# Optimization experiments

Measured on AMD Instinct MI355X. Metric: run time of the kernel, lower is better.

## Reference

```python
import jax, jax.numpy as jnp
import numpy as np

NUM_ITEM = 80000
NUM_USER = 20000
N = NUM_ITEM + NUM_USER
E = 1_000_000
DIM_FEAT = 64
USER_DIM = 128
DIM_ID = 64
SLOPE = 0.01  # F.leaky_relu default negative_slope


def setup_inputs() -> dict:
    key = jax.random.key(0)
    ks = jax.random.split(key, 16)
    s = 0.05
    # self-loop-free random edge list (torch code removes self loops)
    src = jax.random.randint(ks[0], (E,), 0, N)
    off = jax.random.randint(ks[1], (E,), 1, N)
    dst = (src + off) % N
    edge_index = jnp.stack([src, dst]).astype(jnp.int32)
    return {
        "features": jax.random.normal(ks[2], (NUM_ITEM, DIM_FEAT), jnp.float32),
        "user_features": jax.random.normal(ks[3], (NUM_USER, USER_DIM), jnp.float32),
        "id_embedding_weight": jax.random.normal(ks[4], (N, DIM_ID), jnp.float32) * s,
        "user_mlp_w": jax.random.normal(ks[5], (DIM_FEAT, USER_DIM), jnp.float32) * s,
        "user_mlp_b": jnp.zeros((DIM_FEAT,), jnp.float32),
        "gat1_w": jax.random.normal(ks[6], (DIM_FEAT, DIM_FEAT), jnp.float32) * s,
        "lin1_w": jax.random.normal(ks[7], (DIM_ID, DIM_FEAT), jnp.float32) * s,
        "lin1_b": jnp.zeros((DIM_ID,), jnp.float32),
        "g1_w": jax.random.normal(ks[8], (DIM_ID, DIM_FEAT), jnp.float32) * s,
        "g1_b": jnp.zeros((DIM_ID,), jnp.float32),
        "gat2_w": jax.random.normal(ks[9], (DIM_ID, DIM_ID), jnp.float32) * s,
        "lin2_w": jax.random.normal(ks[10], (DIM_ID, DIM_ID), jnp.float32) * s,
        "lin2_b": jnp.zeros((DIM_ID,), jnp.float32),
        "g2_w": jax.random.normal(ks[11], (DIM_ID, DIM_ID), jnp.float32) * s,
        "g2_b": jnp.zeros((DIM_ID,), jnp.float32),
        "edge_index": edge_index,
    }


def leaky_relu(x):
    return jnp.where(x >= 0, x, SLOPE * x)


def graph_gat(x, W, src, dst):
    """GraphGAT layer (MGAT-style): x@W, inner-product attention with
    degree-based sigmoid gate, edge softmax over target nodes, scatter-add."""
    n = x.shape[0]
    xw = x @ W                                   # [N, d_out]
    x_i = xw[dst]                                # gathered target feats [E, d]
    x_j = xw[src]                                # gathered source feats [E, d]
    inner = jnp.sum(x_i * x_j, axis=-1)          # [E]
    deg = jnp.zeros((n,), xw.dtype).at[src].add(1.0)
    dinv = deg[src] ** -0.5                      # deg[src] >= 1 by construction
    gate = jax.nn.sigmoid(dinv * inner)
    logits = inner * gate
    # segment softmax over destination index (PyG softmax)
    m = jax.ops.segment_max(logits, dst, num_segments=n)
    m = jnp.where(jnp.isfinite(m), m, 0.0)
    e = jnp.exp(logits - m[dst])
    z = jax.ops.segment_sum(e, dst, num_segments=n)
    attn = e / (z[dst] + 1e-16)
    msg = x_j * attn[:, None]                    # [E, d]
    return jnp.zeros_like(xw).at[dst].add(msg)   # scatter-add aggr


def reference(features, user_features, id_embedding_weight,
              user_mlp_w, user_mlp_b,
              gat1_w, lin1_w, lin1_b, g1_w, g1_b,
              gat2_w, lin2_w, lin2_b, g2_w, g2_b,
              edge_index):
    src, dst = edge_index[0], edge_index[1]
    user = jnp.tanh(user_features @ user_mlp_w.T + user_mlp_b)
    x = jnp.concatenate([features, user], axis=0)          # [N, dim_feat]
    nrm = jnp.linalg.norm(x, axis=-1, keepdims=True)
    x = x / jnp.maximum(nrm, 1e-12)                        # F.normalize

    # hop 1
    h = leaky_relu(graph_gat(x, gat1_w, src, dst))
    x_hat = leaky_relu(x @ lin1_w.T + lin1_b) + id_embedding_weight
    x1 = leaky_relu(h @ g1_w.T + g1_b + x_hat)

    # hop 2
    h = leaky_relu(graph_gat(x1, gat2_w, src, dst))
    x_hat = leaky_relu(x1 @ lin2_w.T + lin2_b) + id_embedding_weight
    x2 = leaky_relu(h @ g2_w.T + g2_b + x_hat)

    return jnp.concatenate([x1, x2], axis=1)               # [N, 2*dim_id]
```

## Files before the change

kernel.cpp:

```cpp
#include <hip/hip_runtime.h>
#include <hip/hip_bf16.h>
#include <hip/hip_fp16.h>

#define N_ITEM 80000
#define N_USER 20000
#define NN     100000
#define NE     1000000
#define SCAN_T 1024
#define SCAN_TILES ((NN + SCAN_T - 1) / SCAN_T)

typedef __hip_bfloat16 bf16;

__device__ __forceinline__ float b2f(bf16 v) { return __bfloat162float(v); }
__device__ __forceinline__ bf16  f2b(float v) { return __float2bfloat16(v); }
__device__ __forceinline__ float bits2f(unsigned short h) {
    return __uint_as_float(((unsigned)h) << 16);
}
__device__ __forceinline__ float leaky(float v) { return v >= 0.f ? v : 0.01f * v; }

template<typename T>
__device__ __forceinline__ float ldT(const void* p, size_t i);
template<> __device__ __forceinline__ float ldT<float>(const void* p, size_t i) {
    return ((const float*)p)[i];
}
template<> __device__ __forceinline__ float ldT<bf16>(const void* p, size_t i) {
    return b2f(((const bf16*)p)[i]);
}
template<typename T>
__device__ __forceinline__ float4 ldT4(const void* p, size_t i);
template<> __device__ __forceinline__ float4 ldT4<float>(const void* p, size_t i) {
    return *(const float4*)((const float*)p + i);
}
template<> __device__ __forceinline__ float4 ldT4<bf16>(const void* p, size_t i) {
    ushort4 u = *(const ushort4*)((const unsigned short*)p + i);
    return make_float4(bits2f(u.x), bits2f(u.y), bits2f(u.z), bits2f(u.w));
}
template<typename T>
__device__ __forceinline__ void stT4(void* p, size_t i, float4 v);
template<> __device__ __forceinline__ void stT4<float>(void* p, size_t i, float4 v) {
    *(float4*)((float*)p + i) = v;
}
template<> __device__ __forceinline__ void stT4<bf16>(void* p, size_t i, float4 v) {
    bf16 b0 = f2b(v.x), b1 = f2b(v.y), b2 = f2b(v.z), b3 = f2b(v.w);
    ushort4 u = make_ushort4(*(unsigned short*)&b0, *(unsigned short*)&b1,
                             *(unsigned short*)&b2, *(unsigned short*)&b3);
    *(ushort4*)((unsigned short*)p + i) = u;
}
__device__ __forceinline__ float4 ld4f(const float* p, size_t i) {
    return *(const float4*)(p + i);
}
__device__ __forceinline__ float4 ld4b(const unsigned short* p, size_t i) {
    ushort4 u = *(const ushort4*)(p + i);
    return make_float4(bits2f(u.x), bits2f(u.y), bits2f(u.z), bits2f(u.w));
}
__device__ __forceinline__ void st4b(unsigned short* p, size_t i, float4 v) {
    bf16 b0 = f2b(v.x), b1 = f2b(v.y), b2 = f2b(v.z), b3 = f2b(v.w);
    ushort4 u = make_ushort4(*(unsigned short*)&b0, *(unsigned short*)&b1,
                             *(unsigned short*)&b2, *(unsigned short*)&b3);
    *(ushort4*)(p + i) = u;
}
__device__ __forceinline__ float4 ld4h(const unsigned short* p, size_t i) {
    ushort4 u = *(const ushort4*)(p + i);
    __half h0, h1, h2, h3;
    *(unsigned short*)&h0 = u.x; *(unsigned short*)&h1 = u.y;
    *(unsigned short*)&h2 = u.z; *(unsigned short*)&h3 = u.w;
    return make_float4(__half2float(h0), __half2float(h1),
                       __half2float(h2), __half2float(h3));
}
__device__ __forceinline__ void st4h(unsigned short* p, size_t i, float4 v) {
    __half h0 = __float2half(v.x), h1 = __float2half(v.y);
    __half h2 = __float2half(v.z), h3 = __float2half(v.w);
    ushort4 u = make_ushort4(*(unsigned short*)&h0, *(unsigned short*)&h1,
                             *(unsigned short*)&h2, *(unsigned short*)&h3);
    *(ushort4*)(p + i) = u;
}

__device__ __forceinline__ float wred(float v) {
    for (int o = 32; o; o >>= 1) v += __shfl_xor(v, o, 64);
    return v;
}
__device__ __forceinline__ float gred16(float v) {
    for (int o = 8; o; o >>= 1) v += __shfl_xor(v, o, 64);
    return v;
}
__device__ __forceinline__ int wscan(int v, int lane) {
    for (int o = 1; o < 64; o <<= 1) {
        int t = __shfl_up(v, o, 64);
        v += (lane >= o) ? t : 0;
    }
    return v;
}

__global__ void k_detect(const unsigned short* __restrict__ w, int* __restrict__ mode) {
    __shared__ int cnt[256];
    int bad = 0;
    for (int i = threadIdx.x; i < 4096; i += 256) {
        unsigned e = (w[i] >> 7) & 0xFFu;
        bad += (e == 0u || e == 0xFFu) ? 1 : 0;
    }
    cnt[threadIdx.x] = bad;
    __syncthreads();
    if (threadIdx.x == 0) {
        int t = 0;
        for (int k = 0; k < 256; k++) t += cnt[k];
        mode[0] = (t > 0) ? 1 : 0;
    }
}

__global__ void k_prep_w(const void* umw, const void* lw1, const void* gw1,
                         const void* lw2, const void* gw2,
                         float* umwT, float* wT, const int* mode) {
    int t = blockIdx.x * 256 + threadIdx.x;
    bool f32m = (*mode != 0);
    if (t < 8192) {
        int j = t >> 7, k = t & 127;
        float v = f32m ? ldT<float>(umw, t) : ldT<bf16>(umw, t);
        umwT[k * 64 + j] = v;
    } else {
        int u = t - 8192;
        int m = u >> 12;
        int r = u & 4095;
        int j = r >> 6, k = r & 63;
        const void* srcp = (m == 0) ? lw1 : (m == 1) ? gw1 : (m == 2) ? lw2 : gw2;
        float v = f32m ? ldT<float>(srcp, r) : ldT<bf16>(srcp, r);
        wT[m * 4096 + k * 64 + j] = v;
    }
}

__global__ void k_deg(const int* __restrict__ src, const int* __restrict__ dst,
                      int* __restrict__ deg, int* __restrict__ cnt) {
    int e = blockIdx.x * blockDim.x + threadIdx.x;
    if (e < NE) {
        atomicAdd(&deg[src[e]], 1);
        atomicAdd(&cnt[dst[e]], 1);
    }
}

__global__ void k_scan_sum(const int* __restrict__ cnt, const int* __restrict__ deg,
                           float* __restrict__ dinv, int* __restrict__ tsum) {
    __shared__ int wsum[16];
    int i = blockIdx.x * SCAN_T + threadIdx.x;
    int lane = threadIdx.x & 63, wid = threadIdx.x >> 6;
    int v = (i < NN) ? cnt[i] : 0;
    if (i < NN) dinv[i] = rsqrtf((float)max(deg[i], 1));
    float s = wred((float)v);
    if (lane == 0) wsum[wid] = (int)s;
    __syncthreads();
    if (threadIdx.x == 0) {
        int t = 0;
        #pragma unroll
        for (int k = 0; k < 16; k++) t += wsum[k];
        tsum[blockIdx.x] = t;
    }
}

__global__ void k_scan_tiles(const int* __restrict__ tsum, int* __restrict__ toff) {
    __shared__ int wsum[16];
    int lane = threadIdx.x & 63, wid = threadIdx.x >> 6;
    int v = (threadIdx.x < SCAN_TILES) ? tsum[threadIdx.x] : 0;
    int inc = wscan(v, lane);
    if (lane == 63) wsum[wid] = inc;
    __syncthreads();
    if (wid == 0) {
        int ws = (lane < 16) ? wsum[lane] : 0;
        int wi = wscan(ws, lane);
        if (lane < 16) wsum[lane] = wi - ws;
    }
    __syncthreads();
    if (threadIdx.x < SCAN_TILES) toff[threadIdx.x] = inc - v + wsum[wid];
}

__global__ void k_scan_out(const int* __restrict__ cnt, const int* __restrict__ toff,
                           int* __restrict__ csr_off, int* __restrict__ cursor) {
    __shared__ int wsum[16];
    int i = blockIdx.x * SCAN_T + threadIdx.x;
    int lane = threadIdx.x & 63, wid = threadIdx.x >> 6;
    int v = (i < NN) ? cnt[i] : 0;
    int inc = wscan(v, lane);
    if (lane == 63) wsum[wid] = inc;
    __syncthreads();
    if (wid == 0) {
        int ws = (lane < 16) ? wsum[lane] : 0;
        int wi = wscan(ws, lane);
        if (lane < 16) wsum[lane] = wi - ws;
    }
    __syncthreads();
    int excl = inc - v + wsum[wid] + toff[blockIdx.x];
    if (i < NN) { csr_off[i] = excl; cursor[i] = excl; }
    if (i == NN - 1) csr_off[NN] = excl + v;
}

__global__ void k_scatter(const int* __restrict__ src, const int* __restrict__ dst,
                          int* __restrict__ cursor, int* __restrict__ csr_src) {
    int e = blockIdx.x * blockDim.x + threadIdx.x;
    if (e < NE) {
        int pos = atomicAdd(&cursor[dst[e]], 1);
        csr_src[pos] = src[e];
    }
}

template<typename T>
__device__ __forceinline__ void front_items_body(float4* __restrict__ gsW,
                                                 float4* __restrict__ gsL,
                                                 const void* __restrict__ feat,
                                                 const void* __restrict__ Wg,
                                                 const float* __restrict__ lT,
                                                 const void* __restrict__ lb,
                                                 const void* __restrict__ id_emb,
                                                 unsigned short* __restrict__ xw,
                                                 unsigned short* __restrict__ xhat) {
    int lane = threadIdx.x & 63, wid = threadIdx.x >> 6;
    int sl = lane & 15;
    int i = blockIdx.x * 16 + (wid << 2) + (lane >> 4);
    #pragma unroll
    for (int t = 0; t < 4; t++) {
        int idx = threadIdx.x + t * 256;
        gsW[idx] = ldT4<T>(Wg, (size_t)idx * 4);
        gsL[idx] = ld4f(lT, (size_t)idx * 4);
    }
    size_t rb = (size_t)i * 64 + sl * 4;
    float4 v = ldT4<T>(feat, rb);
    float ss = gred16(v.x * v.x + v.y * v.y + v.z * v.z + v.w * v.w);
    float inv = 1.f / fmaxf(sqrtf(ss), 1e-12f);
    float4 xv = make_float4(v.x * inv, v.y * inv, v.z * inv, v.w * inv);
    float4 lb4 = ldT4<T>(lb, sl * 4);
    float4 id4 = ldT4<T>(id_emb, rb);
    __syncthreads();
    float4 accw = make_float4(0.f, 0.f, 0.f, 0.f);
    float4 accl = make_float4(0.f, 0.f, 0.f, 0.f);
    int gbase = lane & 48;
    #pragma unroll
    for (int kk = 0; kk < 16; kk++) {
        int srcl = gbase | kk;
        float xb[4];
        xb[0] = __shfl(xv.x, srcl, 64);
        xb[1] = __shfl(xv.y, srcl, 64);
        xb[2] = __shfl(xv.z, srcl, 64);
        xb[3] = __shfl(xv.w, srcl, 64);
        #pragma unroll
        for (int q = 0; q < 4; q++) {
            int wb = (kk * 4 + q) * 16 + sl;
            float4 w4 = gsW[wb];
            float4 l4 = gsL[wb];
            accw.x += xb[q] * w4.x; accw.y += xb[q] * w4.y;
            accw.z += xb[q] * w4.z; accw.w += xb[q] * w4.w;
            accl.x += xb[q] * l4.x; accl.y += xb[q] * l4.y;
            accl.z += xb[q] * l4.z; accl.w += xb[q] * l4.w;
        }
    }
    st4b(xw, rb, accw);
    float4 xh;
    xh.x = leaky(accl.x + lb4.x) + id4.x;
    xh.y = leaky(accl.y + lb4.y) + id4.y;
    xh.z = leaky(accl.z + lb4.z) + id4.z;
    xh.w = leaky(accl.w + lb4.w) + id4.w;
    st4h(xhat, rb, xh);
}
__global__ void k_front_items(const void* feat, const void* Wg, const float* lT,
                              const void* lb, const void* id_emb,
                              unsigned short* xw, unsigned short* xhat,
                              const int* mode) {
    __shared__ float4 gsW[1024];
    __shared__ float4 gsL[1024];
    if (*mode) front_items_body<float>(gsW, gsL, feat, Wg, lT, lb, id_emb, xw, xhat);
    else       front_items_body<bf16>(gsW, gsL, feat, Wg, lT, lb, id_emb, xw, xhat);
}

template<typename T>
__device__ __forceinline__ void front_users_body(float4* __restrict__ gs,
                                                 const void* __restrict__ uf,
                                                 const float* __restrict__ umwT,
                                                 const void* __restrict__ umb,
                                                 const void* __restrict__ Wg,
                                                 const float* __restrict__ lT,
                                                 const void* __restrict__ lb,
                                                 const void* __restrict__ id_emb,
                                                 unsigned short* __restrict__ xw,
                                                 unsigned short* __restrict__ xhat) {
    int lane = threadIdx.x & 63, wid = threadIdx.x >> 6;
    int sl = lane & 15;
    int u = blockIdx.x * 16 + (wid << 2) + (lane >> 4);
    int i = N_ITEM + u;
    int gbase = lane & 48;
    #pragma unroll
    for (int t = 0; t < 8; t++) {
        int idx = threadIdx.x + t * 256;
        gs[idx] = ld4f(umwT, (size_t)idx * 4);
    }
    __syncthreads();
    size_t ub = (size_t)u * 128;
    float4 acc = ldT4<T>(umb, sl * 4);
    #pragma unroll 4
    for (int k = 0; k < 128; k++) {
        float ufk = ldT<T>(uf, ub + k);
        float4 w4 = gs[k * 16 + sl];
        acc.x += ufk * w4.x; acc.y += ufk * w4.y;
        acc.z += ufk * w4.z; acc.w += ufk * w4.w;
    }
    float4 v = make_float4(tanhf(acc.x), tanhf(acc.y), tanhf(acc.z), tanhf(acc.w));
    float ss = gred16(v.x * v.x + v.y * v.y + v.z * v.z + v.w * v.w);
    float inv = 1.f / fmaxf(sqrtf(ss), 1e-12f);
    float4 xv = make_float4(v.x * inv, v.y * inv, v.z * inv, v.w * inv);
    __syncthreads();
    #pragma unroll
    for (int t = 0; t < 4; t++) {
        int idx = threadIdx.x + t * 256;
        gs[idx] = ldT4<T>(Wg, (size_t)idx * 4);
        gs[idx + 1024] = ld4f(lT, (size_t)idx * 4);
    }
    size_t rb = (size_t)i * 64 + sl * 4;
    float4 lb4 = ldT4<T>(lb, sl * 4);
    float4 id4 = ldT4<T>(id_emb, rb);
    __syncthreads();
    float4 accw = make_float4(0.f, 0.f, 0.f, 0.f);
    float4 accl = make_float4(0.f, 0.f, 0.f, 0.f);
    #pragma unroll
    for (int kk = 0; kk < 16; kk++) {
        int srcl = gbase | kk;
        float xb[4];
        xb[0] = __shfl(xv.x, srcl, 64);
        xb[1] = __shfl(xv.y, srcl, 64);
        xb[2] = __shfl(xv.z, srcl, 64);
        xb[3] = __shfl(xv.w, srcl, 64);
        #pragma unroll
        for (int q = 0; q < 4; q++) {
            int wb = (kk * 4 + q) * 16 + sl;
            float4 w4 = gs[wb];
            float4 l4 = gs[wb + 1024];
            accw.x += xb[q] * w4.x; accw.y += xb[q] * w4.y;
            accw.z += xb[q] * w4.z; accw.w += xb[q] * w4.w;
            accl.x += xb[q] * l4.x; accl.y += xb[q] * l4.y;
            accl.z += xb[q] * l4.z; accl.w += xb[q] * l4.w;
        }
    }
    st4b(xw, rb, accw);
    float4 xh;
    xh.x = leaky(accl.x + lb4.x) + id4.x;
    xh.y = leaky(accl.y + lb4.y) + id4.y;
    xh.z = leaky(accl.z + lb4.z) + id4.z;
    xh.w = leaky(accl.w + lb4.w) + id4.w;
    st4h(xhat, rb, xh);
}
__global__ void k_front_users(const void* uf, const float* umwT, const void* umb,
                              const void* Wg, const float* lT, const void* lb,
                              const void* id_emb,
                              unsigned short* xw, unsigned short* xhat,
                              const int* mode) {
    __shared__ float4 gs[2048];
    if (*mode) front_users_body<float>(gs, uf, umwT, umb, Wg, lT, lb,
                                       id_emb, xw, xhat);
    else       front_users_body<bf16>(gs, uf, umwT, umb, Wg, lT, lb,
                                      id_emb, xw, xhat);
}

template<typename T>
__device__ __forceinline__ void pre_body(float4* __restrict__ gsW,
                                         float4* __restrict__ gsL,
                                         const float* __restrict__ xin,
                                         const void* __restrict__ Wg,
                                         const float* __restrict__ lT,
                                         const void* __restrict__ lb,
                                         const void* __restrict__ id_emb,
                                         unsigned short* __restrict__ xw,
                                         unsigned short* __restrict__ xhat) {
    int lane = threadIdx.x & 63, wid = threadIdx.x >> 6;
    int sl = lane & 15;
    int i = blockIdx.x * 16 + (wid << 2) + (lane >> 4);
    #pragma unroll
    for (int t = 0; t < 4; t++) {
        int idx = threadIdx.x + t * 256;
        gsW[idx] = ldT4<T>(Wg, (size_t)idx * 4);
        gsL[idx] = ld4f(lT, (size_t)idx * 4);
    }
    size_t rb = (size_t)i * 64 + sl * 4;
    float4 xv = ld4f(xin, rb);
    float4 lb4 = ldT4<T>(lb, sl * 4);
    float4 id4 = ldT4<T>(id_emb, rb);
    __syncthreads();
    float4 accw = make_float4(0.f, 0.f, 0.f, 0.f);
    float4 accl = make_float4(0.f, 0.f, 0.f, 0.f);
    int gbase = lane & 48;
    #pragma unroll
    for (int kk = 0; kk < 16; kk++) {
        int srcl = gbase | kk;
        float xb[4];
        xb[0] = __shfl(xv.x, srcl, 64);
        xb[1] = __shfl(xv.y, srcl, 64);
        xb[2] = __shfl(xv.z, srcl, 64);
        xb[3] = __shfl(xv.w, srcl, 64);
        #pragma unroll
        for (int q = 0; q < 4; q++) {
            int wb = (kk * 4 + q) * 16 + sl;
            float4 w4 = gsW[wb];
            float4 l4 = gsL[wb];
            accw.x += xb[q] * w4.x; accw.y += xb[q] * w4.y;
            accw.z += xb[q] * w4.z; accw.w += xb[q] * w4.w;
            accl.x += xb[q] * l4.x; accl.y += xb[q] * l4.y;
            accl.z += xb[q] * l4.z; accl.w += xb[q] * l4.w;
        }
    }
    st4b(xw, rb, accw);
    float4 xh;
    xh.x = leaky(accl.x + lb4.x) + id4.x;
    xh.y = leaky(accl.y + lb4.y) + id4.y;
    xh.z = leaky(accl.z + lb4.z) + id4.z;
    xh.w = leaky(accl.w + lb4.w) + id4.w;
    st4h(xhat, rb, xh);
}
__global__ void k_pre(const float* xin, const void* Wg, const float* lT,
                      const void* lb, const void* id_emb,
                      unsigned short* xw, unsigned short* xhat, const int* mode) {
    __shared__ float4 gsW[1024];
    __shared__ float4 gsL[1024];
    if (*mode) pre_body<float>(gsW, gsL, xin, Wg, lT, lb, id_emb, xw, xhat);
    else       pre_body<bf16>(gsW, gsL, xin, Wg, lT, lb, id_emb, xw, xhat);
}

template<typename T>
__device__ __forceinline__ void gat_body(float4* __restrict__ gs,
                                         const unsigned short* __restrict__ xw,
                                         const unsigned short* __restrict__ xhat,
                                         const int* __restrict__ csr_off,
                                         const int* __restrict__ csr_src,
                                         const float* __restrict__ dinv,
                                         const float* __restrict__ gTg,
                                         const void* gb,
                                         float* __restrict__ xnext, void* out,
                                         int off_out) {
    int lane = threadIdx.x & 63, wid = threadIdx.x >> 6;
    int sl = lane & 15;
    int i = blockIdx.x * 16 + (wid << 2) + (lane >> 4);
    size_t rb = (size_t)i * 64 + sl * 4;
    #pragma unroll
    for (int t = 0; t < 4; t++)
        gs[threadIdx.x + t * 256] = ((const float4*)gTg)[threadIdx.x + t * 256];

    float4 xd = ld4b(xw, rb);
    int e0 = csr_off[i], e1 = csr_off[i + 1];
    int cnt = e1 - e0;
    float m = -1e30f, l = 0.f;
    float4 acc = make_float4(0.f, 0.f, 0.f, 0.f);
    float4 xsA = make_float4(0.f, 0.f, 0.f, 0.f), xsB = xsA;
    float dA = 1.f, dB = 1.f;
    if (cnt > 0) {
        int s0 = csr_src[e0];
        xsA = ld4b(xw, (size_t)s0 * 64 + sl * 4);
        dA = dinv[s0];
    }
    if (cnt > 1) {
        int s1 = csr_src[e0 + 1];
        xsB = ld4b(xw, (size_t)s1 * 64 + sl * 4);
        dB = dinv[s1];
    }
    for (int t = 0; t < cnt; ++t) {
        float4 xs = xsA; float dv = dA;
        xsA = xsB; dA = dB;
        if (t + 2 < cnt) {
            int sn = csr_src[e0 + t + 2];
            xsB = ld4b(xw, (size_t)sn * 64 + sl * 4);
            dB = dinv[sn];
        }
        float p = xd.x * xs.x + xd.y * xs.y + xd.z * xs.z + xd.w * xs.w;
        float inner = gred16(p);
        float gate = 1.f / (1.f + __expf(-dv * inner));
        float logit = inner * gate;
        float mn = fmaxf(m, logit);
        float sc = __expf(m - mn);
        float w  = __expf(logit - mn);
        acc.x = acc.x * sc + w * xs.x;
        acc.y = acc.y * sc + w * xs.y;
        acc.z = acc.z * sc + w * xs.z;
        acc.w = acc.w * sc + w * xs.w;
        l = l * sc + w;
        m = mn;
    }
    float linv = 1.f / (l + 1e-16f);
    float4 hv = make_float4(leaky(acc.x * linv), leaky(acc.y * linv),
                            leaky(acc.z * linv), leaky(acc.w * linv));
    __syncthreads();
    float4 accg = make_float4(0.f, 0.f, 0.f, 0.f);
    int gbase = lane & 48;
    #pragma unroll
    for (int kk = 0; kk < 16; kk++) {
        int srcl = gbase | kk;
        float hb[4];
        hb[0] = __shfl(hv.x, srcl, 64);
        hb[1] = __shfl(hv.y, srcl, 64);
        hb[2] = __shfl(hv.z, srcl, 64);
        hb[3] = __shfl(hv.w, srcl, 64);
        #pragma unroll
        for (int q = 0; q < 4; q++) {
            float4 g4 = gs[(kk * 4 + q) * 16 + sl];
            accg.x += hb[q] * g4.x; accg.y += hb[q] * g4.y;
            accg.z += hb[q] * g4.z; accg.w += hb[q] * g4.w;
        }
    }
    float4 gb4 = ldT4<T>(gb, sl * 4);
    float4 xh4 = ld4h(xhat, rb);
    float4 xn;
    xn.x = leaky(accg.x + gb4.x + xh4.x);
    xn.y = leaky(accg.y + gb4.y + xh4.y);
    xn.z = leaky(accg.z + gb4.z + xh4.z);
    xn.w = leaky(accg.w + gb4.w + xh4.w);
    if (xnext) *(float4*)(xnext + rb) = xn;
    stT4<T>(out, (size_t)i * 128 + off_out + sl * 4, xn);
}
__global__ void k_gat(const unsigned short* xw, const unsigned short* xhat,
                      const int* csr_off, const int* csr_src, const float* dinv,
                      const float* gTg, const void* gb,
                      float* xnext, void* out, int off_out, const int* mode) {
    __shared__ float4 gs[1024];
    if (*mode) gat_body<float>(gs, xw, xhat, csr_off, csr_src, dinv, gTg, gb,
                               xnext, out, off_out);
    else       gat_body<bf16>(gs, xw, xhat, csr_off, csr_src, dinv, gTg, gb,
                              xnext, out, off_out);
}

extern "C" void kernel_launch(void* const* d_in, const int* in_sizes, int n_in,
                              void* d_out, int out_size, void* d_ws, size_t ws_size,
                              hipStream_t stream) {
    const void* feat   = d_in[0];
    const void* uf     = d_in[1];
    const void* id_emb = d_in[2];
    const void* umw    = d_in[3];
    const void* umb    = d_in[4];
    const void* gat1   = d_in[5];
    const void* lin1b  = d_in[7];
    const void* g1b    = d_in[9];
    const void* gat2   = d_in[10];
    const void* lin2b  = d_in[12];
    const void* g2b    = d_in[14];
    const int*  ei     = (const int*)d_in[15];
    const int* src = ei;
    const int* dst = ei + NE;

    int*      mode   = (int*)d_ws;
    int*      deg    = (int*)((char*)d_ws + 16);
    int*      cnt    = deg + NN;
    int*      cursor = cnt + NN;
    int*      csr_off = cursor + NN;
    int*      tsum   = csr_off + NN + 16;
    int*      toff   = tsum + 128;
    float*    dinv   = (float*)(toff + 128);
    float*    umwT   = dinv + NN;
    float*    wT     = umwT + 8192;
    int*      csr_src = (int*)(wT + 4 * 4096);
    float*    buf0   = (float*)(csr_src + NE);
    float*    buf2   = buf0 + (size_t)NN * 64;
    unsigned short* xwb   = (unsigned short*)(buf2 + (size_t)NN * 64);
    unsigned short* xhath = xwb + (size_t)NN * 64;

    k_detect<<<1, 256, 0, stream>>>((const unsigned short*)feat, mode);
    k_prep_w<<<96, 256, 0, stream>>>(umw, d_in[6], d_in[8], d_in[11], d_in[13],
                                     umwT, wT, mode);
    hipMemsetAsync(deg, 0, 2 * NN * 4, stream);
    k_deg<<<(NE + 255) / 256, 256, 0, stream>>>(src, dst, deg, cnt);
    k_scan_sum<<<SCAN_TILES, SCAN_T, 0, stream>>>(cnt, deg, dinv, tsum);
    k_scan_tiles<<<1, SCAN_T, 0, stream>>>(tsum, toff);
    k_scan_out<<<SCAN_TILES, SCAN_T, 0, stream>>>(cnt, toff, csr_off, cursor);
    k_scatter<<<(NE + 255) / 256, 256, 0, stream>>>(src, dst, cursor, csr_src);

    const float* lT1 = wT;
    const float* gT1 = wT + 4096;
    const float* lT2 = wT + 8192;
    const float* gT2 = wT + 12288;

    int nb = NN / 16;

    k_front_items<<<N_ITEM / 16, 256, 0, stream>>>(feat, gat1, lT1, lin1b,
                                                   id_emb, xwb, xhath, mode);
    k_front_users<<<N_USER / 16, 256, 0, stream>>>(uf, umwT, umb, gat1, lT1,
                                                   lin1b, id_emb, xwb, xhath,
                                                   mode);
    k_gat<<<nb, 256, 0, stream>>>(xwb, xhath, csr_off, csr_src, dinv,
                                  gT1, g1b, buf2, d_out, 0, mode);
    k_pre<<<nb, 256, 0, stream>>>(buf2, gat2, lT2, lin2b, id_emb,
                                  xwb, xhath, mode);
    k_gat<<<nb, 256, 0, stream>>>(xwb, xhath, csr_off, csr_src, dinv,
                                  gT2, g2b, nullptr, d_out, 64, mode);
}
```

Baseline: 558.9 us.

## Fuse hop-2 pre-projection into hop-1 GAT kernel with fp16 weights in LDS

The separate pre kernel, which read the hop-1 output x1 from an fp32 buffer, is folded into the first GAT kernel. That kernel now computes x1·gat2 and the lin2 projection from registers, using fp16 copies of both weights staged in shared memory. This removes one launch and the fp32 write and read of x1. Separate ping-pong buffers avoid overwriting xw and xhat while other blocks still read them. In exchange the fused kernel uses more LDS and registers, and the fp16 weights add small rounding error.

```diff
diff --git a/kernel.cpp b/kernel.cpp
--- a/kernel.cpp
+++ b/kernel.cpp
@@ -17,6 +17,10 @@
     return __uint_as_float(((unsigned)h) << 16);
 }
 __device__ __forceinline__ float leaky(float v) { return v >= 0.f ? v : 0.01f * v; }
+__device__ __forceinline__ unsigned short f2h(float v) {
+    __half h = __float2half(v);
+    return *(unsigned short*)&h;
+}
 
 template<typename T>
 __device__ __forceinline__ float ldT(const void* p, size_t i);
@@ -59,19 +63,18 @@
                              *(unsigned short*)&b2, *(unsigned short*)&b3);
     *(ushort4*)(p + i) = u;
 }
-__device__ __forceinline__ float4 ld4h(const unsigned short* p, size_t i) {
-    ushort4 u = *(const ushort4*)(p + i);
+__device__ __forceinline__ float4 cvt4h(ushort4 u) {
     __half h0, h1, h2, h3;
     *(unsigned short*)&h0 = u.x; *(unsigned short*)&h1 = u.y;
     *(unsigned short*)&h2 = u.z; *(unsigned short*)&h3 = u.w;
     return make_float4(__half2float(h0), __half2float(h1),
                        __half2float(h2), __half2float(h3));
 }
+__device__ __forceinline__ float4 ld4h(const unsigned short* p, size_t i) {
+    return cvt4h(*(const ushort4*)(p + i));
+}
 __device__ __forceinline__ void st4h(unsigned short* p, size_t i, float4 v) {
-    __half h0 = __float2half(v.x), h1 = __float2half(v.y);
-    __half h2 = __float2half(v.z), h3 = __float2half(v.w);
-    ushort4 u = make_ushort4(*(unsigned short*)&h0, *(unsigned short*)&h1,
-                             *(unsigned short*)&h2, *(unsigned short*)&h3);
+    ushort4 u = make_ushort4(f2h(v.x), f2h(v.y), f2h(v.z), f2h(v.w));
     *(ushort4*)(p + i) = u;
 }
 
@@ -108,15 +111,17 @@
 }
 
 __global__ void k_prep_w(const void* umw, const void* lw1, const void* gw1,
-                         const void* lw2, const void* gw2,
-                         float* umwT, float* wT, const int* mode) {
+                         const void* lw2, const void* gw2, const void* gat2,
+                         float* umwT, float* wT,
+                         unsigned short* wg2h, unsigned short* lt2h,
+                         const int* mode) {
     int t = blockIdx.x * 256 + threadIdx.x;
     bool f32m = (*mode != 0);
     if (t < 8192) {
         int j = t >> 7, k = t & 127;
         float v = f32m ? ldT<float>(umw, t) : ldT<bf16>(umw, t);
         umwT[k * 64 + j] = v;
-    } else {
+    } else if (t < 24576) {
         int u = t - 8192;
         int m = u >> 12;
         int r = u & 4095;
@@ -124,6 +129,11 @@
         const void* srcp = (m == 0) ? lw1 : (m == 1) ? gw1 : (m == 2) ? lw2 : gw2;
         float v = f32m ? ldT<float>(srcp, r) : ldT<bf16>(srcp, r);
         wT[m * 4096 + k * 64 + j] = v;
+        if (m == 2) lt2h[k * 64 + j] = f2h(v);
+    } else {
+        int r = t - 24576;
+        float v = f32m ? ldT<float>(gat2, r) : ldT<bf16>(gat2, r);
+        wg2h[r] = f2h(v);
     }
 }
 
@@ -354,86 +364,33 @@
 }
 
 template<typename T>
-__device__ __forceinline__ void pre_body(float4* __restrict__ gsW,
-                                         float4* __restrict__ gsL,
-                                         const float* __restrict__ xin,
-                                         const void* __restrict__ Wg,
-                                         const float* __restrict__ lT,
-                                         const void* __restrict__ lb,
-                                         const void* __restrict__ id_emb,
-                                         unsigned short* __restrict__ xw,
-                                         unsigned short* __restrict__ xhat) {
-    int lane = threadIdx.x & 63, wid = threadIdx.x >> 6;
-    int sl = lane & 15;
-    int i = blockIdx.x * 16 + (wid << 2) + (lane >> 4);
-    #pragma unroll
-    for (int t = 0; t < 4; t++) {
-        int idx = threadIdx.x + t * 256;
-        gsW[idx] = ldT4<T>(Wg, (size_t)idx * 4);
-        gsL[idx] = ld4f(lT, (size_t)idx * 4);
-    }
-    size_t rb = (size_t)i * 64 + sl * 4;
-    float4 xv = ld4f(xin, rb);
-    float4 lb4 = ldT4<T>(lb, sl * 4);
-    float4 id4 = ldT4<T>(id_emb, rb);
-    __syncthreads();
-    float4 accw = make_float4(0.f, 0.f, 0.f, 0.f);
-    float4 accl = make_float4(0.f, 0.f, 0.f, 0.f);
-    int gbase = lane & 48;
-    #pragma unroll
-    for (int kk = 0; kk < 16; kk++) {
-        int srcl = gbase | kk;
-        float xb[4];
-        xb[0] = __shfl(xv.x, srcl, 64);
-        xb[1] = __shfl(xv.y, srcl, 64);
-        xb[2] = __shfl(xv.z, srcl, 64);
-        xb[3] = __shfl(xv.w, srcl, 64);
-        #pragma unroll
-        for (int q = 0; q < 4; q++) {
-            int wb = (kk * 4 + q) * 16 + sl;
-            float4 w4 = gsW[wb];
-            float4 l4 = gsL[wb];
-            accw.x += xb[q] * w4.x; accw.y += xb[q] * w4.y;
-            accw.z += xb[q] * w4.z; accw.w += xb[q] * w4.w;
-            accl.x += xb[q] * l4.x; accl.y += xb[q] * l4.y;
-            accl.z += xb[q] * l4.z; accl.w += xb[q] * l4.w;
-        }
-    }
-    st4b(xw, rb, accw);
-    float4 xh;
-    xh.x = leaky(accl.x + lb4.x) + id4.x;
-    xh.y = leaky(accl.y + lb4.y) + id4.y;
-    xh.z = leaky(accl.z + lb4.z) + id4.z;
-    xh.w = leaky(accl.w + lb4.w) + id4.w;
-    st4h(xhat, rb, xh);
-}
-__global__ void k_pre(const float* xin, const void* Wg, const float* lT,
-                      const void* lb, const void* id_emb,
-                      unsigned short* xw, unsigned short* xhat, const int* mode) {
-    __shared__ float4 gsW[1024];
-    __shared__ float4 gsL[1024];
-    if (*mode) pre_body<float>(gsW, gsL, xin, Wg, lT, lb, id_emb, xw, xhat);
-    else       pre_body<bf16>(gsW, gsL, xin, Wg, lT, lb, id_emb, xw, xhat);
-}
-
-template<typename T>
-__device__ __forceinline__ void gat_body(float4* __restrict__ gs,
-                                         const unsigned short* __restrict__ xw,
-                                         const unsigned short* __restrict__ xhat,
-                                         const int* __restrict__ csr_off,
-                                         const int* __restrict__ csr_src,
-                                         const float* __restrict__ dinv,
-                                         const float* __restrict__ gTg,
-                                         const void* gb,
-                                         float* __restrict__ xnext, void* out,
-                                         int off_out) {
+__device__ __forceinline__ void gatf_body(float4* __restrict__ gs,
+                                          ushort4* __restrict__ gsh,
+                                          const unsigned short* __restrict__ xw,
+                                          const unsigned short* __restrict__ xhat,
+                                          const int* __restrict__ csr_off,
+                                          const int* __restrict__ csr_src,
+                                          const float* __restrict__ dinv,
+                                          const float* __restrict__ gTg,
+                                          const void* gb,
+                                          const unsigned short* __restrict__ wg2h,
+                                          const unsigned short* __restrict__ lt2h,
+                                          const void* lb2,
+                                          const void* __restrict__ id_emb,
+                                          void* out,
+                                          unsigned short* __restrict__ xw2,
+                                          unsigned short* __restrict__ xhat2) {
     int lane = threadIdx.x & 63, wid = threadIdx.x >> 6;
     int sl = lane & 15;
     int i = blockIdx.x * 16 + (wid << 2) + (lane >> 4);
     size_t rb = (size_t)i * 64 + sl * 4;
     #pragma unroll
-    for (int t = 0; t < 4; t++)
-        gs[threadIdx.x + t * 256] = ((const float4*)gTg)[threadIdx.x + t * 256];
+    for (int t = 0; t < 4; t++) {
+        int idx = threadIdx.x + t * 256;
+        gs[idx] = ((const float4*)gTg)[idx];
+        gsh[idx] = ((const ushort4*)wg2h)[idx];
+        gsh[idx + 1024] = ((const ushort4*)lt2h)[idx];
+    }
 
     float4 xd = ld4b(xw, rb);
     int e0 = csr_off[i], e1 = csr_off[i + 1];
@@ -502,6 +459,139 @@
     xn.y = leaky(accg.y + gb4.y + xh4.y);
     xn.z = leaky(accg.z + gb4.z + xh4.z);
     xn.w = leaky(accg.w + gb4.w + xh4.w);
+    stT4<T>(out, (size_t)i * 128 + sl * 4, xn);
+    float4 accw = make_float4(0.f, 0.f, 0.f, 0.f);
+    float4 accl = make_float4(0.f, 0.f, 0.f, 0.f);
+    #pragma unroll
+    for (int kk = 0; kk < 16; kk++) {
+        int srcl = gbase | kk;
+        float xb[4];
+        xb[0] = __shfl(xn.x, srcl, 64);
+        xb[1] = __shfl(xn.y, srcl, 64);
+        xb[2] = __shfl(xn.z, srcl, 64);
+        xb[3] = __shfl(xn.w, srcl, 64);
+        #pragma unroll
+        for (int q = 0; q < 4; q++) {
+            int wb = (kk * 4 + q) * 16 + sl;
+            float4 w4 = cvt4h(gsh[wb]);
+            float4 l4 = cvt4h(gsh[wb + 1024]);
+            accw.x += xb[q] * w4.x; accw.y += xb[q] * w4.y;
+            accw.z += xb[q] * w4.z; accw.w += xb[q] * w4.w;
+            accl.x += xb[q] * l4.x; accl.y += xb[q] * l4.y;
+            accl.z += xb[q] * l4.z; accl.w += xb[q] * l4.w;
+        }
+    }
+    st4b(xw2, rb, accw);
+    float4 lb4b = ldT4<T>(lb2, sl * 4);
+    float4 id4 = ldT4<T>(id_emb, rb);
+    float4 xh2;
+    xh2.x = leaky(accl.x + lb4b.x) + id4.x;
+    xh2.y = leaky(accl.y + lb4b.y) + id4.y;
+    xh2.z = leaky(accl.z + lb4b.z) + id4.z;
+    xh2.w = leaky(accl.w + lb4b.w) + id4.w;
+    st4h(xhat2, rb, xh2);
+}
+__global__ void k_gat_fused(const unsigned short* xw, const unsigned short* xhat,
+                            const int* csr_off, const int* csr_src,
+                            const float* dinv, const float* gTg, const void* gb,
+                            const unsigned short* wg2h, const unsigned short* lt2h,
+                            const void* lb2, const void* id_emb, void* out,
+                            unsigned short* xw2, unsigned short* xhat2,
+                            const int* mode) {
+    __shared__ float4 gs[1024];
+    __shared__ ushort4 gsh[2048];
+    if (*mode) gatf_body<float>(gs, gsh, xw, xhat, csr_off, csr_src, dinv, gTg,
+                                gb, wg2h, lt2h, lb2, id_emb, out, xw2, xhat2);
+    else       gatf_body<bf16>(gs, gsh, xw, xhat, csr_off, csr_src, dinv, gTg,
+                               gb, wg2h, lt2h, lb2, id_emb, out, xw2, xhat2);
+}
+
+template<typename T>
+__device__ __forceinline__ void gat_body(float4* __restrict__ gs,
+                                         const unsigned short* __restrict__ xw,
+                                         const unsigned short* __restrict__ xhat,
+                                         const int* __restrict__ csr_off,
+                                         const int* __restrict__ csr_src,
+                                         const float* __restrict__ dinv,
+                                         const float* __restrict__ gTg,
+                                         const void* gb,
+                                         float* __restrict__ xnext, void* out,
+                                         int off_out) {
+    int lane = threadIdx.x & 63, wid = threadIdx.x >> 6;
+    int sl = lane & 15;
+    int i = blockIdx.x * 16 + (wid << 2) + (lane >> 4);
+    size_t rb = (size_t)i * 64 + sl * 4;
+    #pragma unroll
+    for (int t = 0; t < 4; t++)
+        gs[threadIdx.x + t * 256] = ((const float4*)gTg)[threadIdx.x + t * 256];
+
+    float4 xd = ld4b(xw, rb);
+    int e0 = csr_off[i], e1 = csr_off[i + 1];
+    int cnt = e1 - e0;
+    float m = -1e30f, l = 0.f;
+    float4 acc = make_float4(0.f, 0.f, 0.f, 0.f);
+    float4 xsA = make_float4(0.f, 0.f, 0.f, 0.f), xsB = xsA;
+    float dA = 1.f, dB = 1.f;
+    if (cnt > 0) {
+        int s0 = csr_src[e0];
+        xsA = ld4b(xw, (size_t)s0 * 64 + sl * 4);
+        dA = dinv[s0];
+    }
+    if (cnt > 1) {
+        int s1 = csr_src[e0 + 1];
+        xsB = ld4b(xw, (size_t)s1 * 64 + sl * 4);
+        dB = dinv[s1];
+    }
+    for (int t = 0; t < cnt; ++t) {
+        float4 xs = xsA; float dv = dA;
+        xsA = xsB; dA = dB;
+        if (t + 2 < cnt) {
+            int sn = csr_src[e0 + t + 2];
+            xsB = ld4b(xw, (size_t)sn * 64 + sl * 4);
+            dB = dinv[sn];
+        }
+        float p = xd.x * xs.x + xd.y * xs.y + xd.z * xs.z + xd.w * xs.w;
+        float inner = gred16(p);
+        float gate = 1.f / (1.f + __expf(-dv * inner));
+        float logit = inner * gate;
+        float mn = fmaxf(m, logit);
+        float sc = __expf(m - mn);
+        float w  = __expf(logit - mn);
+        acc.x = acc.x * sc + w * xs.x;
+        acc.y = acc.y * sc + w * xs.y;
+        acc.z = acc.z * sc + w * xs.z;
+        acc.w = acc.w * sc + w * xs.w;
+        l = l * sc + w;
+        m = mn;
+    }
+    float linv = 1.f / (l + 1e-16f);
+    float4 hv = make_float4(leaky(acc.x * linv), leaky(acc.y * linv),
+                            leaky(acc.z * linv), leaky(acc.w * linv));
+    __syncthreads();
+    float4 accg = make_float4(0.f, 0.f, 0.f, 0.f);
+    int gbase = lane & 48;
+    #pragma unroll
+    for (int kk = 0; kk < 16; kk++) {
+        int srcl = gbase | kk;
+        float hb[4];
+        hb[0] = __shfl(hv.x, srcl, 64);
+        hb[1] = __shfl(hv.y, srcl, 64);
+        hb[2] = __shfl(hv.z, srcl, 64);
+        hb[3] = __shfl(hv.w, srcl, 64);
+        #pragma unroll
+        for (int q = 0; q < 4; q++) {
+            float4 g4 = gs[(kk * 4 + q) * 16 + sl];
+            accg.x += hb[q] * g4.x; accg.y += hb[q] * g4.y;
+            accg.z += hb[q] * g4.z; accg.w += hb[q] * g4.w;
+        }
+    }
+    float4 gb4 = ldT4<T>(gb, sl * 4);
+    float4 xh4 = ld4h(xhat, rb);
+    float4 xn;
+    xn.x = leaky(accg.x + gb4.x + xh4.x);
+    xn.y = leaky(accg.y + gb4.y + xh4.y);
+    xn.z = leaky(accg.z + gb4.z + xh4.z);
+    xn.w = leaky(accg.w + gb4.w + xh4.w);
     if (xnext) *(float4*)(xnext + rb) = xn;
     stT4<T>(out, (size_t)i * 128 + off_out + sl * 4, xn);
 }
@@ -544,15 +634,17 @@
     float*    dinv   = (float*)(toff + 128);
     float*    umwT   = dinv + NN;
     float*    wT     = umwT + 8192;
-    int*      csr_src = (int*)(wT + 4 * 4096);
-    float*    buf0   = (float*)(csr_src + NE);
-    float*    buf2   = buf0 + (size_t)NN * 64;
-    unsigned short* xwb   = (unsigned short*)(buf2 + (size_t)NN * 64);
+    unsigned short* wg2h = (unsigned short*)(wT + 4 * 4096);
+    unsigned short* lt2h = wg2h + 4096;
+    int*      csr_src = (int*)(lt2h + 4096);
+    unsigned short* xwb   = (unsigned short*)(csr_src + NE);
     unsigned short* xhath = xwb + (size_t)NN * 64;
+    unsigned short* xwb2   = xhath + (size_t)NN * 64;
+    unsigned short* xhath2 = xwb2 + (size_t)NN * 64;
 
     k_detect<<<1, 256, 0, stream>>>((const unsigned short*)feat, mode);
-    k_prep_w<<<96, 256, 0, stream>>>(umw, d_in[6], d_in[8], d_in[11], d_in[13],
-                                     umwT, wT, mode);
+    k_prep_w<<<112, 256, 0, stream>>>(umw, d_in[6], d_in[8], d_in[11], d_in[13],
+                                      gat2, umwT, wT, wg2h, lt2h, mode);
     hipMemsetAsync(deg, 0, 2 * NN * 4, stream);
     k_deg<<<(NE + 255) / 256, 256, 0, stream>>>(src, dst, deg, cnt);
     k_scan_sum<<<SCAN_TILES, SCAN_T, 0, stream>>>(cnt, deg, dinv, tsum);
@@ -562,7 +654,6 @@
 
     const float* lT1 = wT;
     const float* gT1 = wT + 4096;
-    const float* lT2 = wT + 8192;
     const float* gT2 = wT + 12288;
 
     int nb = NN / 16;
@@ -572,10 +663,9 @@
     k_front_users<<<N_USER / 16, 256, 0, stream>>>(uf, umwT, umb, gat1, lT1,
                                                    lin1b, id_emb, xwb, xhath,
                                                    mode);
-    k_gat<<<nb, 256, 0, stream>>>(xwb, xhath, csr_off, csr_src, dinv,
-                                  gT1, g1b, buf2, d_out, 0, mode);
-    k_pre<<<nb, 256, 0, stream>>>(buf2, gat2, lT2, lin2b, id_emb,
-                                  xwb, xhath, mode);
-    k_gat<<<nb, 256, 0, stream>>>(xwb, xhath, csr_off, csr_src, dinv,
+    k_gat_fused<<<nb, 256, 0, stream>>>(xwb, xhath, csr_off, csr_src, dinv,
+                                        gT1, g1b, wg2h, lt2h, lin2b, id_emb,
+                                        d_out, xwb2, xhath2, mode);
+    k_gat<<<nb, 256, 0, stream>>>(xwb2, xhath2, csr_off, csr_src, dinv,
                                   gT2, g2b, nullptr, d_out, 64, mode);
 }
```

New measurement: 566.2 us. Within noise of the previous version (+1.3%).
